# Performance work log

Hardware: AMD Instinct MI355X
Metric: run time of the kernel (lower is better)

## Reference

```python
import jax, jax.numpy as jnp
import numpy as np

D_MODEL = 1024
N_HEADS = 16
D_K = D_MODEL // N_HEADS
D_FF = 4096
EPS = 1e-6


def setup_inputs() -> dict:
    key = jax.random.key(0)
    ks = jax.random.split(key, 10)
    B, S = 2, 2048
    s = 0.02
    return {
        "x": jax.random.normal(ks[0], (B, S, D_MODEL), dtype=jnp.float32),
        "mask": jnp.ones((1, 1, S, S), dtype=jnp.int32),
        "wq": jax.random.normal(ks[1], (D_MODEL, D_MODEL), dtype=jnp.float32) * s,
        "wk": jax.random.normal(ks[2], (D_MODEL, D_MODEL), dtype=jnp.float32) * s,
        "wv": jax.random.normal(ks[3], (D_MODEL, D_MODEL), dtype=jnp.float32) * s,
        "wo": jax.random.normal(ks[4], (D_MODEL, D_MODEL), dtype=jnp.float32) * s,
        "w1": jax.random.normal(ks[5], (D_FF, D_MODEL), dtype=jnp.float32) * s,
        "b1": jnp.zeros((D_FF,), dtype=jnp.float32),
        "w2": jax.random.normal(ks[6], (D_MODEL, D_FF), dtype=jnp.float32) * s,
        "b2": jnp.zeros((D_MODEL,), dtype=jnp.float32),
        "ln1_a": jnp.ones((D_MODEL,), dtype=jnp.float32),
        "ln1_b": jnp.zeros((D_MODEL,), dtype=jnp.float32),
        "ln2_a": jnp.ones((D_MODEL,), dtype=jnp.float32),
        "ln2_b": jnp.zeros((D_MODEL,), dtype=jnp.float32),
    }


def layer_norm(x, alpha, bias):
    # Faithful to the torch module: unbiased std (ddof=1), eps added to std (not var)
    mean = jnp.mean(x, axis=-1, keepdims=True)
    std = jnp.std(x, axis=-1, keepdims=True, ddof=1)
    return alpha * (x - mean) / (std + EPS) + bias


def mha(h, mask, wq, wk, wv, wo):
    B, S, _ = h.shape
    # nn.Linear: y = x @ W.T
    q = (h @ wq.T).reshape(B, S, N_HEADS, D_K).transpose(0, 2, 1, 3)  # bhsd
    k = (h @ wk.T).reshape(B, S, N_HEADS, D_K).transpose(0, 2, 1, 3)
    v = (h @ wv.T).reshape(B, S, N_HEADS, D_K).transpose(0, 2, 1, 3)
    scores = jnp.einsum('bhqd,bhkd->bhqk', q, k) / jnp.sqrt(jnp.float32(D_K))
    scores = jnp.where(mask == 0, jnp.float32(-1e9), scores)
    attn = jax.nn.softmax(scores, axis=-1)  # dropout is identity in eval
    out = jnp.einsum('bhqk,bhkd->bhqd', attn, v)
    out = out.transpose(0, 2, 1, 3).reshape(B, S, D_MODEL)
    return out @ wo.T


def reference(x, mask, wq, wk, wv, wo, w1, b1, w2, b2, ln1_a, ln1_b, ln2_a, ln2_b):
    # Residual 1: pre-norm self-attention
    x = x + mha(layer_norm(x, ln1_a, ln1_b), mask, wq, wk, wv, wo)
    # Residual 2: pre-norm FFN
    h = layer_norm(x, ln2_a, ln2_b)
    ff = jax.nn.relu(h @ w1.T + b1) @ w2.T + b2
    return x + ff
```

## Files before the change

### kernel.cpp

```cpp
#include <hip/hip_runtime.h>
#include <math.h>

#define D_MODEL 1024
#define DFF 4096
#define SEQ 2048
#define ROWS 4096
#define EPS 1e-6f
#define QSCALE 0.1803368801111243f

typedef __bf16 bf16_t;
typedef __bf16 bf16x8 __attribute__((ext_vector_type(8)));
typedef __bf16 bf16x4 __attribute__((ext_vector_type(4)));
typedef float f32x4 __attribute__((ext_vector_type(4)));

typedef const __attribute__((address_space(1))) uint32_t* gas_ptr;
typedef __attribute__((address_space(3))) uint32_t* las_ptr;

__device__ __forceinline__ void gld_lds16(const void* g, void* l) {
    __builtin_amdgcn_global_load_lds((gas_ptr)g, (las_ptr)l, 16, 0, 0);
}

__device__ __forceinline__ float exp2_fast(float x) {
    float r;
    __asm__ volatile("v_exp_f32 %0, %1" : "=v"(r) : "v"(x));
    return r;
}

__device__ __forceinline__ int xcd_swz(int orig, int nwg) {
    const int q = nwg >> 3, r = nwg & 7, xcd = orig & 7, loc = orig >> 3;
    return (xcd < r ? xcd * (q + 1) : r * (q + 1) + (xcd - r) * q) + loc;
}

#define BAR() asm volatile("s_barrier" ::: "memory")

template<int EPI>
__global__ __launch_bounds__(512, 2) void gemm256(
        const bf16_t* __restrict__ A, const bf16_t* __restrict__ B,
        void* __restrict__ Cv, int Ktile, int lda, int ldb, int ldc,
        const float* __restrict__ bias, size_t zstride,
        bf16_t* __restrict__ vt,
        const float* __restrict__ cwo, const float* __restrict__ cw1,
        const float* __restrict__ cw2, bf16_t* __restrict__ dwo,
        bf16_t* __restrict__ dw1, bf16_t* __restrict__ dw2) {
    const int tid = threadIdx.x, l = tid & 63, w = tid >> 6;

    if (EPI == 5 && (int)blockIdx.x >= 192) {
        const int sid = blockIdx.x - 192;
        const size_t base = (size_t)sid * 147456;
        for (int it = 0; it < 72; ++it) {
            const size_t idx = base + ((size_t)it * 512 + tid) * 4;
            const float* s; bf16_t* d; size_t off;
            if (idx < (size_t)(1u << 20))      { s = cwo; d = dwo; off = idx; }
            else if (idx < (size_t)(5u << 20)) { s = cw1; d = dw1; off = idx - (1u << 20); }
            else                               { s = cw2; d = dw2; off = idx - (5u << 20); }
            float4 v = *(const float4*)(s + off);
            bf16x4 o = { (bf16_t)v.x, (bf16_t)v.y, (bf16_t)v.z, (bf16_t)v.w };
            *(bf16x4*)(d + off) = o;
        }
        return;
    }

    extern __shared__ bf16_t sm[];
    bf16_t* smA = sm;
    bf16_t* smB = sm + 32768;
    const int wm = w >> 2, wn = w & 3;
    const int flatid = (EPI == 5) ? (int)blockIdx.x
                                  : (int)(blockIdx.y * gridDim.x + blockIdx.x);
    const int ntile = (EPI == 5) ? 192 : (int)(gridDim.x * gridDim.y);
    const int nyq = ((EPI == 5) ? 16 : (int)gridDim.y) << 2;
    const int swz = xcd_swz(flatid, ntile);
    const int inb = swz % nyq;
    const int bm = (inb >> 2) << 8;
    const int bn = (((swz / nyq) << 2) + (inb & 3)) << 8;
    const int koff = blockIdx.z * Ktile;
    const int NT = Ktile >> 6;

    const int srow = (w << 3) + (l >> 3);
    const int scol = ((l & 7) ^ (l >> 3)) << 3;
    const bf16_t* gAs = A + (size_t)(bm + srow) * lda + koff + scol;
    const bf16_t* gBs = B + (size_t)(bn + srow) * ldb + koff + scol;
    const int sb = (w << 3) << 6;

    const int cs0 = (((l >> 4)    ) ^ (l & 7)) << 3;
    const int cs1 = (((l >> 4) + 4) ^ (l & 7)) << 3;
    const int rA = (wm << 7) + (l & 15);
    const int rB = (wn << 6) + (l & 15);

    f32x4 acc[8][4] = {};
    bf16x8 af[4][2], bl[2][2], bh[2][2];

    auto stA = [&](int kt, int h, int buf) {
        const bf16_t* g = gAs + (kt << 6);
        bf16_t* s = smA + (buf << 14) + ((h << 7) << 6) + sb;
        gld_lds16(g + (size_t)(h << 7) * lda, s);
        gld_lds16(g + (size_t)((h << 7) + 64) * lda, s + 4096);
    };
    auto stB = [&](int kt, int h, int buf) {
        const bf16_t* g = gBs + (kt << 6);
        bf16_t* s = smB + (buf << 14) + ((h << 7) << 6) + sb;
        gld_lds16(g + (size_t)(h << 7) * ldb, s);
        gld_lds16(g + (size_t)((h << 7) + 64) * ldb, s + 4096);
    };
    auto ldA = [&](int buf, int mh) {
        const bf16_t* base = smA + (buf << 14) + (rA + mh * 64) * 64;
        #pragma unroll
        for (int mf = 0; mf < 4; ++mf) {
            af[mf][0] = *(const bf16x8*)(base + mf * 1024 + cs0);
            af[mf][1] = *(const bf16x8*)(base + mf * 1024 + cs1);
        }
    };
    auto ldB = [&](int buf, int nh, bf16x8 (*bq)[2]) {
        const bf16_t* base = smB + (buf << 14) + (rB + nh * 32) * 64;
        #pragma unroll
        for (int nf = 0; nf < 2; ++nf) {
            bq[nf][0] = *(const bf16x8*)(base + nf * 1024 + cs0);
            bq[nf][1] = *(const bf16x8*)(base + nf * 1024 + cs1);
        }
    };
    auto mm = [&](bf16x8 (*bq)[2], int mo, int no) {
        __builtin_amdgcn_s_setprio(1);
        #pragma unroll
        for (int kk = 0; kk < 2; ++kk)
            #pragma unroll
            for (int mf = 0; mf < 4; ++mf)
                #pragma unroll
                for (int nf = 0; nf < 2; ++nf)
                    acc[mo + mf][no + nf] = __builtin_amdgcn_mfma_f32_16x16x32_bf16(
                        af[mf][kk], bq[nf][kk], acc[mo + mf][no + nf], 0, 0, 0);
        __builtin_amdgcn_s_setprio(0);
    };

    stA(0, 0, 0); stA(0, 1, 0); stB(0, 0, 0); stB(0, 1, 0);
    if (NT > 1) {
        stB(1, 0, 1); stA(1, 0, 1);
        asm volatile("s_waitcnt vmcnt(4)" ::: "memory");
    } else {
        asm volatile("s_waitcnt vmcnt(0)" ::: "memory");
    }
    BAR();
    ldA(0, 0); ldB(0, 0, bl); ldB(0, 1, bh);

    auto period = [&](int T, int buf) {
        if (T + 1 < NT) stA(T + 1, 1, buf ^ 1);
        BAR();
        mm(bl, 0, 0);
        BAR();
        if (T + 1 < NT) stB(T + 1, 1, buf ^ 1);
        BAR();
        mm(bh, 0, 2);
        ldA(buf, 1);
        BAR();
        if (T + 2 < NT) stB(T + 2, 0, buf);
        BAR();
        mm(bh, 4, 2);
        BAR();
        if (T + 2 < NT) stA(T + 2, 0, buf);
        if (T < NT - 2)       asm volatile("s_waitcnt vmcnt(4)" ::: "memory");
        else if (T == NT - 2) asm volatile("s_waitcnt vmcnt(0)" ::: "memory");
        BAR();
        mm(bl, 4, 0);
        if (T + 1 < NT) {
            ldA(buf ^ 1, 0);
            ldB(buf ^ 1, 0, bl);
            ldB(buf ^ 1, 1, bh);
        }
        BAR();
    };

    for (int T = 0; T < NT; T += 2) { period(T, 0); period(T + 1, 1); }

    const int r0 = bm + (wm << 7) + ((l >> 4) << 2);
    const int c0 = bn + (wn << 6) + (l & 15);
    #pragma unroll
    for (int mf = 0; mf < 8; ++mf) {
        #pragma unroll
        for (int r = 0; r < 4; ++r) {
            const int row = r0 + mf * 16 + r;
            #pragma unroll
            for (int nf = 0; nf < 4; ++nf) {
                const int col = c0 + nf * 16;
                float v = acc[mf][nf][r];
                if (EPI == 1) {
                    ((float*)Cv)[blockIdx.z * zstride + (size_t)row * ldc + col] = v;
                } else if (EPI == 3) {
                    v = fmaxf(v + bias[col], 0.f);
                    ((bf16_t*)Cv)[(size_t)row * ldc + col] = (bf16_t)v;
                } else {
                    if (col < 2048) {
                        ((bf16_t*)Cv)[(size_t)row * ldc + col] = (bf16_t)v;
                    } else {
                        vt[(size_t)(row >> 11) * (1024 * 2048)
                           + (size_t)(col - 2048) * 2048 + (row & 2047)] = (bf16_t)v;
                    }
                }
            }
        }
    }
}

__global__ __launch_bounds__(256) void combine4(
        const float* __restrict__ p, const float* __restrict__ bias,
        const float* __restrict__ res, float* __restrict__ out) {
    const size_t Z = (size_t)4096 * 1024;
    const size_t i = ((size_t)blockIdx.x * 256 + threadIdx.x) * 4;
    float4 a = *(const float4*)(p + i);
    float4 b = *(const float4*)(p + Z + i);
    float4 c = *(const float4*)(p + 2 * Z + i);
    float4 d = *(const float4*)(p + 3 * Z + i);
    float4 r = *(const float4*)(res + i);
    float4 o;
    o.x = (a.x + b.x) + (c.x + d.x) + r.x;
    o.y = (a.y + b.y) + (c.y + d.y) + r.y;
    o.z = (a.z + b.z) + (c.z + d.z) + r.z;
    o.w = (a.w + b.w) + (c.w + d.w) + r.w;
    if (bias) {
        const int col = (int)(i & 1023);
        o.x += bias[col]; o.y += bias[col + 1];
        o.z += bias[col + 2]; o.w += bias[col + 3];
    }
    *(float4*)(out + i) = o;
}

__global__ __launch_bounds__(256) void combine_ln(
        const float* __restrict__ p, const float* __restrict__ res,
        float* __restrict__ x2, const float* __restrict__ lna,
        const float* __restrict__ lnb, bf16_t* __restrict__ lnout) {
    const size_t Z = (size_t)4096 * 1024;
    const int row = blockIdx.x;
    const int tid = threadIdx.x;
    const size_t base = (size_t)row * 1024 + tid * 4;
    float4 a = *(const float4*)(p + base);
    float4 b = *(const float4*)(p + Z + base);
    float4 c = *(const float4*)(p + 2 * Z + base);
    float4 d = *(const float4*)(p + 3 * Z + base);
    float4 r = *(const float4*)(res + base);
    float v[4] = { (a.x + b.x) + (c.x + d.x) + r.x,
                   (a.y + b.y) + (c.y + d.y) + r.y,
                   (a.z + b.z) + (c.z + d.z) + r.z,
                   (a.w + b.w) + (c.w + d.w) + r.w };
    *(float4*)(x2 + base) = *(float4*)v;

    float lsum = (v[0] + v[1]) + (v[2] + v[3]);
    #pragma unroll
    for (int off = 32; off; off >>= 1) lsum += __shfl_down(lsum, off);
    __shared__ float sm4[4];
    const int wid = tid >> 6, lane = tid & 63;
    if (!lane) sm4[wid] = lsum;
    __syncthreads();
    const float mean = (sm4[0] + sm4[1] + sm4[2] + sm4[3]) * (1.0f / D_MODEL);
    float d2 = 0.f;
    #pragma unroll
    for (int j = 0; j < 4; ++j) { float dd = v[j] - mean; d2 += dd * dd; }
    #pragma unroll
    for (int off = 32; off; off >>= 1) d2 += __shfl_down(d2, off);
    __syncthreads();
    if (!lane) sm4[wid] = d2;
    __syncthreads();
    const float var = (sm4[0] + sm4[1] + sm4[2] + sm4[3]) * (1.0f / (D_MODEL - 1));
    const float inv = 1.0f / (sqrtf(var) + EPS);
    const int cc = tid * 4;
    bf16x4 ob = { (bf16_t)(lna[cc]     * (v[0] - mean) * inv + lnb[cc]),
                  (bf16_t)(lna[cc + 1] * (v[1] - mean) * inv + lnb[cc + 1]),
                  (bf16_t)(lna[cc + 2] * (v[2] - mean) * inv + lnb[cc + 2]),
                  (bf16_t)(lna[cc + 3] * (v[3] - mean) * inv + lnb[cc + 3]) };
    *(bf16x4*)(lnout + base) = ob;
}

__global__ __launch_bounds__(256) void wconv_ln(
        const float* __restrict__ wq, const float* __restrict__ wk,
        const float* __restrict__ wv, bf16_t* __restrict__ wqkv_b,
        const float* __restrict__ x, const float* __restrict__ lna,
        const float* __restrict__ lnb, bf16_t* __restrict__ lnout) {
    const int blk = blockIdx.x;
    const int tid = threadIdx.x;
    if (blk >= 3072) {
        const int row = blk - 3072;
        const float* xr = x + (size_t)row * D_MODEL;
        bf16_t* yr = lnout + (size_t)row * D_MODEL;
        float v[4];
        #pragma unroll
        for (int j = 0; j < 4; ++j) v[j] = xr[tid + 256 * j];
        float lsum = v[0] + v[1] + v[2] + v[3];
        #pragma unroll
        for (int off = 32; off; off >>= 1) lsum += __shfl_down(lsum, off);
        __shared__ float sm4[4];
        const int wid = tid >> 6, lane = tid & 63;
        if (!lane) sm4[wid] = lsum;
        __syncthreads();
        const float mean = (sm4[0] + sm4[1] + sm4[2] + sm4[3]) * (1.0f / D_MODEL);
        float d2 = 0.f;
        #pragma unroll
        for (int j = 0; j < 4; ++j) { float d = v[j] - mean; d2 += d * d; }
        #pragma unroll
        for (int off = 32; off; off >>= 1) d2 += __shfl_down(d2, off);
        __syncthreads();
        if (!lane) sm4[wid] = d2;
        __syncthreads();
        const float var = (sm4[0] + sm4[1] + sm4[2] + sm4[3]) * (1.0f / (D_MODEL - 1));
        const float inv = 1.0f / (sqrtf(var) + EPS);
        #pragma unroll
        for (int j = 0; j < 4; ++j) {
            const int c = tid + 256 * j;
            yr[c] = (bf16_t)(lna[c] * (v[j] - mean) * inv + lnb[c]);
        }
        return;
    }
    const float* s; size_t off; float scale = 1.f;
    if (blk < 1024)      { s = wq; off = blk;        scale = QSCALE; }
    else if (blk < 2048) { s = wk; off = blk; }
    else                 { s = wv; off = blk - 1024; }
    const size_t i = off * 1024 + tid * 4;
    const size_t si = (blk < 1024 ? (size_t)blk
                      : blk < 2048 ? (size_t)(blk - 1024)
                                   : (size_t)(blk - 2048)) * 1024 + tid * 4;
    float4 v = *(const float4*)(s + si);
    bf16x4 o = { (bf16_t)(v.x * scale), (bf16_t)(v.y * scale),
                 (bf16_t)(v.z * scale), (bf16_t)(v.w * scale) };
    *(bf16x4*)(wqkv_b + (blk < 2048 ? i : (size_t)(blk - 2048 + 2048) * 1024 + tid * 4)) = o;
}

__global__ __launch_bounds__(512, 4) void flash_attn(
        const bf16_t* __restrict__ qkv, const bf16_t* __restrict__ vt,
        bf16_t* __restrict__ attn) {
    const int orig = blockIdx.y * gridDim.x + blockIdx.x;
    const int swz = ((orig & 7) << 6) + (orig >> 3);
    const int qt = swz & 15, z = swz >> 4;
    const int b = z >> 4, h = z & 15;
    const int tid = threadIdx.x, lane = tid & 63, wave = tid >> 6;
    const int a15 = lane & 15, g4 = lane >> 4;

    extern __shared__ __align__(16) bf16_t dsm[];
    bf16_t* smK = dsm;
    bf16_t* smV = dsm + 12288;
    bf16_t* myP = dsm + 24576 + wave * (16 * 68);

    const bf16_t* Qb = qkv + (size_t)(b * 2048 + qt * 128) * 3072 + h * 64;
    const bf16_t* Kb = qkv + (size_t)(b * 2048) * 3072 + 1024 + h * 64;
    const bf16_t* Vb = vt + (size_t)b * 1024 * 2048 + (size_t)(h * 64) * 2048;

    bf16x8 qf[2];
    #pragma unroll
    for (int c = 0; c < 2; ++c)
        qf[c] = *(const bf16x8*)(Qb + (size_t)(wave * 16 + a15) * 3072
                                 + c * 32 + g4 * 8);

    f32x4 oacc[4] = {};
    float l0 = 0.f;

    auto stage = [&](int kt, int buf) {
        #pragma unroll
        for (int u = 0; u < 2; ++u) {
            const int tk = wave * 2 + u;
            if (tk < 8) {
                const int i = tk >> 1, c = tk & 1;
                gld_lds16(Kb + (size_t)(kt * 64 + i * 16 + a15) * 3072 + c * 32 + g4 * 8,
                          smK + buf * 4096 + tk * 512);
            } else {
                const int tv = tk - 8, t = tv >> 1, c = tv & 1;
                gld_lds16(Vb + (size_t)(t * 16 + a15) * 2048 + kt * 64 + c * 32 + g4 * 8,
                          smV + buf * 4096 + tv * 512);
            }
        }
    };

    stage(0, 0); stage(1, 1);
    asm volatile("s_waitcnt vmcnt(2)" ::: "memory");
    BAR();

    int cur = 0;
    for (int kt = 0; kt < 32; ++kt) {
        const int nx2 = cur == 0 ? 2 : cur - 1;
        if (kt + 2 < 32) stage(kt + 2, nx2);

        f32x4 sacc[4] = {};
        __builtin_amdgcn_s_setprio(1);
        #pragma unroll
        for (int i = 0; i < 4; ++i) {
            bf16x8 k0 = *(const bf16x8*)(smK + cur * 4096 + (i * 2 + 0) * 512 + lane * 8);
            bf16x8 k1 = *(const bf16x8*)(smK + cur * 4096 + (i * 2 + 1) * 512 + lane * 8);
            sacc[i] = __builtin_amdgcn_mfma_f32_16x16x32_bf16(k0, qf[0], sacc[i], 0, 0, 0);
            sacc[i] = __builtin_amdgcn_mfma_f32_16x16x32_bf16(k1, qf[1], sacc[i], 0, 0, 0);
        }
        __builtin_amdgcn_s_setprio(0);

        #pragma unroll
        for (int i = 0; i < 4; ++i) {
            const float p0 = exp2_fast(sacc[i][0]);
            const float p1 = exp2_fast(sacc[i][1]);
            const float p2 = exp2_fast(sacc[i][2]);
            const float p3 = exp2_fast(sacc[i][3]);
            l0 += (p0 + p1) + (p2 + p3);
            bf16x4 pb = { (bf16_t)p0, (bf16_t)p1, (bf16_t)p2, (bf16_t)p3 };
            *(bf16x4*)(myP + a15 * 68 + i * 16 + g4 * 4) = pb;
        }
        __asm__ __volatile__("s_waitcnt lgkmcnt(0)" ::: "memory");

        #pragma unroll
        for (int c = 0; c < 2; ++c) {
            bf16x8 pf = *(const bf16x8*)(myP + a15 * 68 + c * 32 + g4 * 8);
            __builtin_amdgcn_s_setprio(1);
            #pragma unroll
            for (int t = 0; t < 4; ++t) {
                bf16x8 av = *(const bf16x8*)(smV + cur * 4096 + (t * 2 + c) * 512 + lane * 8);
                oacc[t] = __builtin_amdgcn_mfma_f32_16x16x32_bf16(av, pf, oacc[t], 0, 0, 0);
            }
            __builtin_amdgcn_s_setprio(0);
        }

        if (kt < 30)       asm volatile("s_waitcnt vmcnt(2)" ::: "memory");
        else if (kt == 30) asm volatile("s_waitcnt vmcnt(0)" ::: "memory");
        if (kt < 31) BAR();
        cur = cur == 2 ? 0 : cur + 1;
    }

    l0 += __shfl_xor(l0, 16); l0 += __shfl_xor(l0, 32);
    const float inv = 1.f / l0;
    const int q = qt * 128 + wave * 16 + a15;
    bf16_t* orow = attn + (size_t)(b * 2048 + q) * 1024 + h * 64;
    #pragma unroll
    for (int t = 0; t < 4; ++t) {
        bf16x4 ov = { (bf16_t)(oacc[t][0] * inv), (bf16_t)(oacc[t][1] * inv),
                      (bf16_t)(oacc[t][2] * inv), (bf16_t)(oacc[t][3] * inv) };
        *(bf16x4*)(orow + t * 16 + g4 * 4) = ov;
    }
}

extern "C" void kernel_launch(void* const* d_in, const int* in_sizes, int n_in,
                              void* d_out, int out_size, void* d_ws, size_t ws_size,
                              hipStream_t stream) {
    const float* x    = (const float*)d_in[0];
    const float* wq   = (const float*)d_in[2];
    const float* wk   = (const float*)d_in[3];
    const float* wv   = (const float*)d_in[4];
    const float* wo   = (const float*)d_in[5];
    const float* w1   = (const float*)d_in[6];
    const float* b1   = (const float*)d_in[7];
    const float* w2   = (const float*)d_in[8];
    const float* b2   = (const float*)d_in[9];
    const float* ln1a = (const float*)d_in[10];
    const float* ln1bb= (const float*)d_in[11];
    const float* ln2a = (const float*)d_in[12];
    const float* ln2bb= (const float*)d_in[13];
    float* out = (float*)d_out;

    char* W = (char*)d_ws;
    bf16_t* wqkv_b = (bf16_t*)(W);
    bf16_t* wo_b   = (bf16_t*)(W + (6u   << 20));
    bf16_t* w1_b   = (bf16_t*)(W + (8u   << 20));
    bf16_t* w2_b   = (bf16_t*)(W + (16u  << 20));
    float*  x2     = (float*) (W + (24u  << 20));
    bf16_t* ln2_b  = (bf16_t*)(W + (40u  << 20));
    bf16_t* ff1_b  = (bf16_t*)(W + (48u  << 20));
    float*  parts  = (float*) (W + (80u  << 20));
    bf16_t* qkv_b  = (bf16_t*)(W + (80u  << 20));
    bf16_t* vt     = (bf16_t*)(W + (104u << 20));
    bf16_t* ln1_b  = (bf16_t*)(W + (144u << 20));
    bf16_t* attn_b = ln1_b;

    const size_t Z4 = (size_t)4096 * 1024;
    dim3 blk(256), blk5(512);

    wconv_ln<<<7168, blk, 0, stream>>>(wq, wk, wv, wqkv_b,
                                       x, ln1a, ln1bb, ln1_b);

    gemm256<5><<<dim3(256), blk5, 131072, stream>>>(
        ln1_b, wqkv_b, qkv_b, 1024, 1024, 1024, 3072, nullptr, 0, vt,
        wo, w1, w2, wo_b, w1_b, w2_b);

    flash_attn<<<dim3(16, 32), blk5, 66560, stream>>>(qkv_b, vt, attn_b);

    gemm256<1><<<dim3(4, 16, 4), blk5, 131072, stream>>>(
        attn_b, wo_b, parts, 256, 1024, 1024, 1024, nullptr, Z4, nullptr,
        nullptr, nullptr, nullptr, nullptr, nullptr, nullptr);
    combine_ln<<<ROWS, blk, 0, stream>>>(parts, x, x2, ln2a, ln2bb, ln2_b);

    gemm256<3><<<dim3(16, 16), blk5, 131072, stream>>>(
        ln2_b, w1_b, ff1_b, 1024, 1024, 1024, 4096, b1, 0, nullptr,
        nullptr, nullptr, nullptr, nullptr, nullptr, nullptr);

    gemm256<1><<<dim3(4, 16, 4), blk5, 131072, stream>>>(
        ff1_b, w2_b, parts, 1024, 4096, 4096, 1024, nullptr, Z4, nullptr,
        nullptr, nullptr, nullptr, nullptr, nullptr, nullptr);
    combine4<<<4096, blk, 0, stream>>>(parts, b2, x2, out);
}
```

Measured before the change: 374.9 us.

## Replace split-K GEMMs with 128x128-tile GEMM fusing residual and bias epilogue

The out-projection and FFN2 GEMMs used 256x256 tiles with 4-way split-K, writing fp32 partials that a separate combine kernel summed. A new 128x128-tile GEMM (256 blocks, full K per block) adds the residual and bias in its epilogue, which removes the partial buffers and the combine passes. Layer norm 2 becomes a standalone kernel that reads x2. This saves roughly 64MB of partial-sum traffic per GEMM and two kernels' worth of work. In exchange each block runs a longer K loop with smaller tiles and less data reuse.

```diff
diff --git a/kernel.cpp b/kernel.cpp
--- a/kernel.cpp
+++ b/kernel.cpp
@@ -180,9 +180,7 @@
             for (int nf = 0; nf < 4; ++nf) {
                 const int col = c0 + nf * 16;
                 float v = acc[mf][nf][r];
-                if (EPI == 1) {
-                    ((float*)Cv)[blockIdx.z * zstride + (size_t)row * ldc + col] = v;
-                } else if (EPI == 3) {
+                if (EPI == 3) {
                     v = fmaxf(v + bias[col], 0.f);
                     ((bf16_t*)Cv)[(size_t)row * ldc + col] = (bf16_t)v;
                 } else {
@@ -198,48 +196,116 @@
     }
 }
 
-__global__ __launch_bounds__(256) void combine4(
-        const float* __restrict__ p, const float* __restrict__ bias,
-        const float* __restrict__ res, float* __restrict__ out) {
-    const size_t Z = (size_t)4096 * 1024;
-    const size_t i = ((size_t)blockIdx.x * 256 + threadIdx.x) * 4;
-    float4 a = *(const float4*)(p + i);
-    float4 b = *(const float4*)(p + Z + i);
-    float4 c = *(const float4*)(p + 2 * Z + i);
-    float4 d = *(const float4*)(p + 3 * Z + i);
-    float4 r = *(const float4*)(res + i);
-    float4 o;
-    o.x = (a.x + b.x) + (c.x + d.x) + r.x;
-    o.y = (a.y + b.y) + (c.y + d.y) + r.y;
-    o.z = (a.z + b.z) + (c.z + d.z) + r.z;
-    o.w = (a.w + b.w) + (c.w + d.w) + r.w;
-    if (bias) {
-        const int col = (int)(i & 1023);
-        o.x += bias[col]; o.y += bias[col + 1];
-        o.z += bias[col + 2]; o.w += bias[col + 3];
-    }
-    *(float4*)(out + i) = o;
-}
-
-__global__ __launch_bounds__(256) void combine_ln(
-        const float* __restrict__ p, const float* __restrict__ res,
-        float* __restrict__ x2, const float* __restrict__ lna,
+__global__ __launch_bounds__(512, 4) void gemm128f(
+        const bf16_t* __restrict__ A, const bf16_t* __restrict__ B,
+        float* __restrict__ out, int Ktile, int lda, int ldb,
+        const float* __restrict__ bias, const float* __restrict__ res) {
+    extern __shared__ bf16_t sm[];
+    bf16_t* smA = sm;
+    bf16_t* smB = sm + 16384;
+    const int tid = threadIdx.x, l = tid & 63, w = tid >> 6;
+    const int wm = w >> 2, wn = w & 3;
+    const int flat = blockIdx.y * gridDim.x + blockIdx.x;
+    const int swz = xcd_swz(flat, gridDim.x * gridDim.y);
+    const int bm = (swz >> 3) << 7, bn = (swz & 7) << 7;
+    const int NT = Ktile >> 6;
+
+    const int srow = (w << 3) + (l >> 3);
+    const int scol = ((l & 7) ^ (l >> 3)) << 3;
+    const bf16_t* gAs = A + (size_t)(bm + srow) * lda + scol;
+    const bf16_t* gBs = B + (size_t)(bn + srow) * ldb + scol;
+    const int sb = w << 9;
+
+    const int cs0 = (((l >> 4)    ) ^ (l & 7)) << 3;
+    const int cs1 = (((l >> 4) + 4) ^ (l & 7)) << 3;
+
+    f32x4 acc[4][2] = {};
+    bf16x8 a0[4], a1[4], b0[2], b1[2];
+
+    auto stA = [&](int kt, int h, int buf) {
+        gld_lds16(gAs + (size_t)(h << 6) * lda + (kt << 6),
+                  smA + (buf << 13) + (h << 12) + sb);
+    };
+    auto stB = [&](int kt, int h, int buf) {
+        gld_lds16(gBs + (size_t)(h << 6) * ldb + (kt << 6),
+                  smB + (buf << 13) + (h << 12) + sb);
+    };
+    auto ldAk = [&](int buf, bf16x8* a, int cs) {
+        const bf16_t* base = smA + (buf << 13) + (wm << 12) + (l & 15) * 64;
+        #pragma unroll
+        for (int mf = 0; mf < 4; ++mf)
+            a[mf] = *(const bf16x8*)(base + mf * 1024 + cs);
+    };
+    auto ldBk = [&](int buf, bf16x8* b, int cs) {
+        const bf16_t* base = smB + (buf << 13) + ((wn >> 1) << 12)
+                             + (((wn & 1) << 5) + (l & 15)) * 64;
+        #pragma unroll
+        for (int nf = 0; nf < 2; ++nf)
+            b[nf] = *(const bf16x8*)(base + nf * 1024 + cs);
+    };
+    auto mm8 = [&](bf16x8* a, bf16x8* b) {
+        __builtin_amdgcn_s_setprio(1);
+        #pragma unroll
+        for (int mf = 0; mf < 4; ++mf)
+            #pragma unroll
+            for (int nf = 0; nf < 2; ++nf)
+                acc[mf][nf] = __builtin_amdgcn_mfma_f32_16x16x32_bf16(
+                    a[mf], b[nf], acc[mf][nf], 0, 0, 0);
+        __builtin_amdgcn_s_setprio(0);
+    };
+
+    stA(0, 0, 0); stA(0, 1, 0); stB(0, 0, 0); stB(0, 1, 0);
+    if (NT > 1) {
+        stB(1, 0, 1); stA(1, 0, 1);
+        asm volatile("s_waitcnt vmcnt(2)" ::: "memory");
+    } else {
+        asm volatile("s_waitcnt vmcnt(0)" ::: "memory");
+    }
+    BAR();
+    ldAk(0, a0, cs0); ldBk(0, b0, cs0);
+
+    for (int T = 0; T < NT; ++T) {
+        const int buf = T & 1;
+        if (T + 1 < NT) { stA(T + 1, 1, buf ^ 1); stB(T + 1, 1, buf ^ 1); }
+        BAR();
+        mm8(a0, b0);
+        ldAk(buf, a1, cs1); ldBk(buf, b1, cs1);
+        BAR();
+        if (T + 2 < NT) { stB(T + 2, 0, buf); stA(T + 2, 0, buf); }
+        if (T < NT - 2)       asm volatile("s_waitcnt vmcnt(2)" ::: "memory");
+        else if (T == NT - 2) asm volatile("s_waitcnt vmcnt(0)" ::: "memory");
+        BAR();
+        mm8(a1, b1);
+        if (T + 1 < NT) { ldAk(buf ^ 1, a0, cs0); ldBk(buf ^ 1, b0, cs0); }
+        BAR();
+    }
+
+    const int r0 = bm + (wm << 6) + ((l >> 4) << 2);
+    const int c0 = bn + (wn << 5) + (l & 15);
+    #pragma unroll
+    for (int mf = 0; mf < 4; ++mf) {
+        #pragma unroll
+        for (int r = 0; r < 4; ++r) {
+            const int row = r0 + mf * 16 + r;
+            #pragma unroll
+            for (int nf = 0; nf < 2; ++nf) {
+                const int col = c0 + nf * 16;
+                float v = acc[mf][nf][r] + res[(size_t)row * 1024 + col];
+                if (bias) v += bias[col];
+                out[(size_t)row * 1024 + col] = v;
+            }
+        }
+    }
+}
+
+__global__ __launch_bounds__(256) void ln2_k(
+        const float* __restrict__ x2, const float* __restrict__ lna,
         const float* __restrict__ lnb, bf16_t* __restrict__ lnout) {
-    const size_t Z = (size_t)4096 * 1024;
     const int row = blockIdx.x;
     const int tid = threadIdx.x;
     const size_t base = (size_t)row * 1024 + tid * 4;
-    float4 a = *(const float4*)(p + base);
-    float4 b = *(const float4*)(p + Z + base);
-    float4 c = *(const float4*)(p + 2 * Z + base);
-    float4 d = *(const float4*)(p + 3 * Z + base);
-    float4 r = *(const float4*)(res + base);
-    float v[4] = { (a.x + b.x) + (c.x + d.x) + r.x,
-                   (a.y + b.y) + (c.y + d.y) + r.y,
-                   (a.z + b.z) + (c.z + d.z) + r.z,
-                   (a.w + b.w) + (c.w + d.w) + r.w };
-    *(float4*)(x2 + base) = *(float4*)v;
-
+    float4 r = *(const float4*)(x2 + base);
+    float v[4] = { r.x, r.y, r.z, r.w };
     float lsum = (v[0] + v[1]) + (v[2] + v[3]);
     #pragma unroll
     for (int off = 32; off; off >>= 1) lsum += __shfl_down(lsum, off);
@@ -451,13 +517,11 @@
     float*  x2     = (float*) (W + (24u  << 20));
     bf16_t* ln2_b  = (bf16_t*)(W + (40u  << 20));
     bf16_t* ff1_b  = (bf16_t*)(W + (48u  << 20));
-    float*  parts  = (float*) (W + (80u  << 20));
     bf16_t* qkv_b  = (bf16_t*)(W + (80u  << 20));
     bf16_t* vt     = (bf16_t*)(W + (104u << 20));
     bf16_t* ln1_b  = (bf16_t*)(W + (144u << 20));
     bf16_t* attn_b = ln1_b;
 
-    const size_t Z4 = (size_t)4096 * 1024;
     dim3 blk(256), blk5(512);
 
     wconv_ln<<<7168, blk, 0, stream>>>(wq, wk, wv, wqkv_b,
@@ -469,17 +533,15 @@
 
     flash_attn<<<dim3(16, 32), blk5, 66560, stream>>>(qkv_b, vt, attn_b);
 
-    gemm256<1><<<dim3(4, 16, 4), blk5, 131072, stream>>>(
-        attn_b, wo_b, parts, 256, 1024, 1024, 1024, nullptr, Z4, nullptr,
-        nullptr, nullptr, nullptr, nullptr, nullptr, nullptr);
-    combine_ln<<<ROWS, blk, 0, stream>>>(parts, x, x2, ln2a, ln2bb, ln2_b);
+    gemm128f<<<dim3(8, 32), blk5, 65536, stream>>>(
+        attn_b, wo_b, x2, 1024, 1024, 1024, nullptr, x);
+
+    ln2_k<<<ROWS, blk, 0, stream>>>(x2, ln2a, ln2bb, ln2_b);
 
     gemm256<3><<<dim3(16, 16), blk5, 131072, stream>>>(
         ln2_b, w1_b, ff1_b, 1024, 1024, 1024, 4096, b1, 0, nullptr,
         nullptr, nullptr, nullptr, nullptr, nullptr, nullptr);
 
-    gemm256<1><<<dim3(4, 16, 4), blk5, 131072, stream>>>(
-        ff1_b, w2_b, parts, 1024, 4096, 4096, 1024, nullptr, Z4, nullptr,
-        nullptr, nullptr, nullptr, nullptr, nullptr, nullptr);
-    combine4<<<4096, blk, 0, stream>>>(parts, b2, x2, out);
-}
+    gemm128f<<<dim3(8, 32), blk5, 65536, stream>>>(
+        ff1_b, w2_b, out, 4096, 4096, 4096, b2, x2);
+}
```

New measurement: 369.4 us. Within noise of the previous version (-1.4%).
